# Optimization experiments

Measured on AMD Instinct MI355X. Metric: run time of the kernel, lower is better.

The kernel has to match this reference:

```python
import jax, jax.numpy as jnp
import numpy as np

B, T, D, H, O = 64, 512, 256, 1024, 1


def setup_inputs() -> dict:
    key = jax.random.key(0)
    ks = jax.random.split(key, 11)
    s_in = 1.0 / np.sqrt(H)
    def u(k, shape):
        return jax.random.uniform(k, shape, jnp.float32, -s_in, s_in)
    return {
        "x": jax.random.normal(ks[0], (B, T, D), jnp.float32),
        "w_ih_0": u(ks[1], (4 * H, D)),
        "w_hh_0": u(ks[2], (4 * H, H)),
        "b_ih_0": u(ks[3], (4 * H,)),
        "b_hh_0": u(ks[4], (4 * H,)),
        "w_ih_1": u(ks[5], (4 * H, H)),
        "w_hh_1": u(ks[6], (4 * H, H)),
        "b_ih_1": u(ks[7], (4 * H,)),
        "b_hh_1": u(ks[8], (4 * H,)),
        "w_lin": u(ks[9], (O, H)),
        "b_lin": u(ks[10], (O,)),
    }


def _lstm_layer(x, w_ih, w_hh, b_ih, b_hh):
    # x: [B, T, Din] -> h_seq: [B, T, H]. PyTorch gate order: i, f, g, o.
    # Precompute input projections for all timesteps (one big GEMM).
    xp = jnp.einsum("btd,gd->tbg", x, w_ih) + b_ih + b_hh  # [T, B, 4H]
    h0 = jnp.zeros((x.shape[0], w_hh.shape[1]), x.dtype)
    c0 = jnp.zeros_like(h0)

    def step(carry, xp_t):
        h, c = carry
        gates = xp_t + h @ w_hh.T  # [B, 4H]
        i, f, g, o = jnp.split(gates, 4, axis=-1)
        i = jax.nn.sigmoid(i)
        f = jax.nn.sigmoid(f)
        g = jnp.tanh(g)
        o = jax.nn.sigmoid(o)
        c = f * c + i * g
        h = o * jnp.tanh(c)
        return (h, c), h

    (_, _), h_seq = jax.lax.scan(step, (h0, c0), xp)  # h_seq: [T, B, H]
    return jnp.transpose(h_seq, (1, 0, 2))  # [B, T, H]


def reference(x, w_ih_0, w_hh_0, b_ih_0, b_hh_0,
              w_ih_1, w_hh_1, b_ih_1, b_hh_1, w_lin, b_lin):
    h1 = _lstm_layer(x, w_ih_0, w_hh_0, b_ih_0, b_hh_0)
    h2 = _lstm_layer(h1, w_ih_1, w_hh_1, b_ih_1, b_hh_1)
    return h2[:, -1, :] @ w_lin.T + b_lin  # [B, O]
```

## Files before the change

### kernel.cpp

```cpp
#include <hip/hip_runtime.h>


#define T_STEPS 512
#define NWG 256
#define LDS_W     131072
#define LDS_GBUF  (64 * 33 * 4)
#define LDS_CBUF  (64 * 9 * 4)
#define LDS_OFFS  (32 * 4)
#define SMEM_BYTES (LDS_W + LDS_GBUF + LDS_CBUF + LDS_OFFS)

typedef int v2i  __attribute__((ext_vector_type(2)));
typedef int v4i  __attribute__((ext_vector_type(4)));
typedef int v16i __attribute__((ext_vector_type(16)));

__device__ __forceinline__ v16i zero16() {
    v16i z;
#pragma unroll
    for (int i = 0; i < 16; ++i) z[i] = 0;
    return z;
}

__device__ __forceinline__ void load_f16_nw(const char* b0p, v4i* o) {
    const char* b1p = b0p + 4096;
    const char* b2p = b0p + 8192;
    const char* b3p = b0p + 12288;
    asm volatile(
        "global_load_dwordx4 %0, %16, off sc0 sc1\n\t"
        "global_load_dwordx4 %1, %16, off offset:16 sc0 sc1\n\t"
        "global_load_dwordx4 %2, %16, off offset:2048 sc0 sc1\n\t"
        "global_load_dwordx4 %3, %16, off offset:2064 sc0 sc1\n\t"
        "global_load_dwordx4 %4, %17, off sc0 sc1\n\t"
        "global_load_dwordx4 %5, %17, off offset:16 sc0 sc1\n\t"
        "global_load_dwordx4 %6, %17, off offset:2048 sc0 sc1\n\t"
        "global_load_dwordx4 %7, %17, off offset:2064 sc0 sc1\n\t"
        "global_load_dwordx4 %8, %18, off sc0 sc1\n\t"
        "global_load_dwordx4 %9, %18, off offset:16 sc0 sc1\n\t"
        "global_load_dwordx4 %10, %18, off offset:2048 sc0 sc1\n\t"
        "global_load_dwordx4 %11, %18, off offset:2064 sc0 sc1\n\t"
        "global_load_dwordx4 %12, %19, off sc0 sc1\n\t"
        "global_load_dwordx4 %13, %19, off offset:16 sc0 sc1\n\t"
        "global_load_dwordx4 %14, %19, off offset:2048 sc0 sc1\n\t"
        "global_load_dwordx4 %15, %19, off offset:2064 sc0 sc1"
        : "=&v"(o[0]), "=&v"(o[1]), "=&v"(o[2]), "=&v"(o[3]),
          "=&v"(o[4]), "=&v"(o[5]), "=&v"(o[6]), "=&v"(o[7]),
          "=&v"(o[8]), "=&v"(o[9]), "=&v"(o[10]), "=&v"(o[11]),
          "=&v"(o[12]), "=&v"(o[13]), "=&v"(o[14]), "=&v"(o[15])
        : "v"(b0p), "v"(b1p), "v"(b2p), "v"(b3p)
        : "memory");
}

#define WAIT_BIND(cntstr, b)                                                   \
    asm volatile("s_waitcnt vmcnt(" cntstr ")"                                 \
        : "+v"((b)[0]), "+v"((b)[1]), "+v"((b)[2]), "+v"((b)[3]),              \
          "+v"((b)[4]), "+v"((b)[5]), "+v"((b)[6]), "+v"((b)[7]),              \
          "+v"((b)[8]), "+v"((b)[9]), "+v"((b)[10]), "+v"((b)[11]),            \
          "+v"((b)[12]), "+v"((b)[13]), "+v"((b)[14]), "+v"((b)[15])           \
        :: "memory")

__device__ __forceinline__ void st16_wt(void* p, v4i v) {
    asm volatile("global_store_dwordx4 %0, %1, off sc0 sc1" :: "v"(p), "v"(v) : "memory");
}
__device__ __forceinline__ void waitcnt0() {
    asm volatile("s_waitcnt vmcnt(0)" ::: "memory");
}

__device__ __forceinline__ void split_a(v4i A0, v4i A1, v4i& HI, v4i& LO) {
    HI.x = (int)__builtin_amdgcn_perm((unsigned)A0.y, (unsigned)A0.x, 0x07050301u);
    HI.y = (int)__builtin_amdgcn_perm((unsigned)A0.w, (unsigned)A0.z, 0x07050301u);
    HI.z = (int)__builtin_amdgcn_perm((unsigned)A1.y, (unsigned)A1.x, 0x07050301u);
    HI.w = (int)__builtin_amdgcn_perm((unsigned)A1.w, (unsigned)A1.z, 0x07050301u);
    LO.x = (int)(__builtin_amdgcn_perm((unsigned)A0.y, (unsigned)A0.x, 0x06040200u) ^ 0x80808080u);
    LO.y = (int)(__builtin_amdgcn_perm((unsigned)A0.w, (unsigned)A0.z, 0x06040200u) ^ 0x80808080u);
    LO.z = (int)(__builtin_amdgcn_perm((unsigned)A1.y, (unsigned)A1.x, 0x06040200u) ^ 0x80808080u);
    LO.w = (int)(__builtin_amdgcn_perm((unsigned)A1.w, (unsigned)A1.z, 0x06040200u) ^ 0x80808080u);
}

__device__ __forceinline__ void consume8(const v4i* hb, const char* wbase,
                                         v16i& ahh, v16i& amid)
{
#pragma unroll
    for (int s = 0; s < 8; ++s) {
        v4i HI, LO; split_a(hb[2 * s], hb[2 * s + 1], HI, LO);
        v4i BH = *(const v4i*)(wbase + s * 2048);
        v4i BL = *(const v4i*)(wbase + s * 2048 + 1024);
        ahh  = __builtin_amdgcn_mfma_i32_32x32x32_i8(HI, BH, ahh, 0, 0, 0);
        amid = __builtin_amdgcn_mfma_i32_32x32x32_i8(HI, BL, amid, 0, 0, 0);
        amid = __builtin_amdgcn_mfma_i32_32x32x32_i8(LO, BH, amid, 0, 0, 0);
    }
}

__device__ __forceinline__ void kstep(const short* __restrict__ ap,
                                      const char* __restrict__ wl,
                                      v16i& ahh, v16i& amid)
{
    v4i A0 = *(const v4i*)ap;
    v4i A1 = *(const v4i*)(ap + 8);
    v4i HI, LO; split_a(A0, A1, HI, LO);
    v4i BH = *(const v4i*)wl;
    v4i BL = *(const v4i*)(wl + 1024);
    ahh  = __builtin_amdgcn_mfma_i32_32x32x32_i8(HI, BH, ahh, 0, 0, 0);
    amid = __builtin_amdgcn_mfma_i32_32x32x32_i8(HI, BL, amid, 0, 0, 0);
    amid = __builtin_amdgcn_mfma_i32_32x32x32_i8(LO, BH, amid, 0, 0, 0);
}

__global__ void quant_x(const float* __restrict__ x, short* __restrict__ xq, int n)
{
    int i = blockIdx.x * 256 + threadIdx.x;
    if (i < n) {
        float v = x[i] * 2048.f;
        v = fminf(fmaxf(v, -32767.f), 32767.f);
        xq[i] = (short)__float2int_rn(v);
    }
}

__global__ void quant_w(const float* __restrict__ wih0, const float* __restrict__ whh0,
                        const float* __restrict__ wih1, const float* __restrict__ whh1,
                        char* __restrict__ wimg)
{
    int gid = blockIdx.x * 256 + threadIdx.x;
    if (gid >= 256 * 64 * 64) return;
    int lane = gid & 63;
    int s    = (gid >> 6) & 63;
    int wg   = gid >> 12;
    int layer = wg >> 7, nblk = wg & 127;
    int col = nblk * 32 + (lane & 31);
    int ro  = (col & 3) * 1024 + (col >> 2);
    int k0  = s * 32 + (lane >> 5) * 16;
    char* dst = wimg + (size_t)wg * LDS_W + s * 2048 + lane * 16;
#pragma unroll
    for (int j = 0; j < 16; ++j) {
        int k = k0 + j;
        float w = 0.f;
        if (layer == 0) {
            if (k < 256)       w = wih0[ro * 256 + k];
            else if (k < 1280) w = whh0[ro * 1024 + (k - 256)];
        } else {
            if (k < 1024)      w = wih1[ro * 1024 + k];
            else               w = whh1[ro * 1024 + (k - 1024)];
        }
        int q  = __float2int_rn(w * 524288.f);
        int hi = (q + 128) >> 8;
        int lo = q - (hi << 8);
        dst[j]        = (char)hi;
        dst[1024 + j] = (char)lo;
    }
}

__global__ void __launch_bounds__(128) lstm_main(
    const short* __restrict__ xq, const char* __restrict__ wimg,
    const float* __restrict__ bih0, const float* __restrict__ bhh0,
    const float* __restrict__ bih1, const float* __restrict__ bhh1,
    short* __restrict__ h0q, short* __restrict__ h2q,
    float* __restrict__ h2f, unsigned* gslots, unsigned* gbcast)
{
    extern __shared__ char smem[];
    char*  wlds = smem;
    float* gbuf = (float*)(smem + LDS_W);
    float* cbuf = (float*)(smem + LDS_W + LDS_GBUF);
    float* offs = (float*)(smem + LDS_W + LDS_GBUF + LDS_CBUF);

    const int wg    = blockIdx.x;
    const int layer = wg >> 7;
    const int nblk  = wg & 127;
    const int tid   = threadIdx.x;
    const int lane  = tid & 63;
    const int RB    = tid >> 6;
    const float inv30 = 9.313225746154785e-10f;
    const float inv33 = 1.1641532182693481e-10f;

    {
        const v4i* src = (const v4i*)(wimg + (size_t)wg * LDS_W);
        v4i* dst = (v4i*)wlds;
        for (int i = tid; i < LDS_W / 16; i += 128) dst[i] = src[i];
    }
    for (int i = tid; i < 64 * 9; i += 128) cbuf[i] = 0.f;
    __syncthreads();

    if (tid < 32) {
        const int c  = tid;
        const int ns = (layer == 0) ? 40 : 64;
        int cs_x = 0, cs_h = 0;
        for (int s = 0; s < ns; ++s) {
            int sum = 0;
#pragma unroll
            for (int half = 0; half < 2; ++half) {
                const signed char* ph = (const signed char*)(wlds + s * 2048 + (half * 32 + c) * 16);
#pragma unroll
                for (int j = 0; j < 16; ++j)
                    sum += 256 * (int)ph[j] + (int)ph[1024 + j];
            }
            if (layer == 0 && s < 8) cs_x += sum; else cs_h += sum;
        }
        const int col = nblk * 32 + c;
        const int ro  = (col & 3) * 1024 + (col >> 2);
        const float bias = (layer == 0) ? (bih0[ro] + bhh0[ro]) : (bih1[ro] + bhh1[ro]);
        float off = 128.f * (float)cs_h * inv33 + bias;
        if (layer == 0) off += 128.f * (float)cs_x * inv30;
        offs[c] = off;
    }
    __syncthreads();

    const int mrow = RB * 32 + (lane & 31);
    const int ksub = (lane >> 5) * 16;
    const int j0   = nblk * 8;
    const int sj   = j0 >> 5;
    const int hbj  = (j0 >> 4) & 1;
    const int inj  = (j0 & 15) * 2;

    for (int p = 0; p <= T_STEPS; ++p) {
        const bool active = (layer == 0) ? (p < T_STEPS) : (p >= 1);

        float px[16];
        if (layer == 0 && active) {
            v16i ax = zero16(), mx = zero16();
            const short* axp = xq + ((size_t)mrow * 512 + p) * 256 + ksub;
#pragma unroll
            for (int s = 0; s < 8; ++s)
                kstep(axp + s * 32, wlds + s * 2048 + lane * 16, ax, mx);
#pragma unroll
            for (int r = 0; r < 16; ++r)
                px[r] = ((float)ax[r] * 65536.f + (float)mx[r] * 256.f) * inv30;
        }

        if (p > 0) {
            const unsigned pp = (unsigned)p;
            if (wg == 0) {
                const unsigned* s0 = gslots + (tid * 2) * 16;
                const unsigned* s1 = s0 + 16;
                while (__hip_atomic_load(s0, __ATOMIC_RELAXED, __HIP_MEMORY_SCOPE_AGENT) < pp)
                    __builtin_amdgcn_s_sleep(1);
                while (__hip_atomic_load(s1, __ATOMIC_RELAXED, __HIP_MEMORY_SCOPE_AGENT) < pp)
                    __builtin_amdgcn_s_sleep(1);
                __syncthreads();
                __hip_atomic_store(gbcast + (tid * 2) * 16, pp, __ATOMIC_RELAXED, __HIP_MEMORY_SCOPE_AGENT);
                __hip_atomic_store(gbcast + (tid * 2 + 1) * 16, pp, __ATOMIC_RELAXED, __HIP_MEMORY_SCOPE_AGENT);
            } else {
                if (tid == 0) {
                    while (__hip_atomic_load(gbcast + wg * 16, __ATOMIC_RELAXED, __HIP_MEMORY_SCOPE_AGENT) < pp)
                        __builtin_amdgcn_s_sleep(1);
                }
            }
            __syncthreads();
            asm volatile("" ::: "memory");
        }

        if (active) {
            const char* f0 = (const char*)(h0q + ((p + 1) & 1) * 65536)
                           + RB * 65536 + lane * 32;
            float gates[16];
            v16i ahh = zero16(), amid = zero16();
            v4i b0[16], b1[16];
            if (layer == 0) {
                if (p > 0) {
                    waitcnt0();
                    const char* W = wlds + lane * 16;
                    load_f16_nw(f0, b0);
                    load_f16_nw(f0 + 16384, b1);
                    WAIT_BIND("16", b0); consume8(b0, W + 8 * 2048, ahh, amid);
                    load_f16_nw(f0 + 32768, b0);
                    WAIT_BIND("16", b1); consume8(b1, W + 16 * 2048, ahh, amid);
                    load_f16_nw(f0 + 49152, b1);
                    WAIT_BIND("16", b0); consume8(b0, W + 24 * 2048, ahh, amid);
                    WAIT_BIND("0", b1);  consume8(b1, W + 32 * 2048, ahh, amid);
                }
#pragma unroll
                for (int r = 0; r < 16; ++r)
                    gates[r] = px[r]
                             + ((float)ahh[r] * 65536.f + (float)amid[r] * 256.f) * inv33
                             + offs[lane & 31];
            } else {
                const char* f2 = (const char*)(h2q + ((p + 1) & 1) * 65536)
                               + RB * 65536 + lane * 32;
                waitcnt0();
                const char* W = wlds + lane * 16;
                load_f16_nw(f0, b0);
                load_f16_nw(f0 + 16384, b1);
                WAIT_BIND("16", b0); consume8(b0, W, ahh, amid);
                load_f16_nw(f0 + 32768, b0);
                WAIT_BIND("16", b1); consume8(b1, W + 8 * 2048, ahh, amid);
                load_f16_nw(f0 + 49152, b1);
                WAIT_BIND("16", b0); consume8(b0, W + 16 * 2048, ahh, amid);
                load_f16_nw(f2, b0);
                WAIT_BIND("16", b1); consume8(b1, W + 24 * 2048, ahh, amid);
                load_f16_nw(f2 + 16384, b1);
                WAIT_BIND("16", b0); consume8(b0, W + 32 * 2048, ahh, amid);
                load_f16_nw(f2 + 32768, b0);
                WAIT_BIND("16", b1); consume8(b1, W + 40 * 2048, ahh, amid);
                load_f16_nw(f2 + 49152, b1);
                WAIT_BIND("16", b0); consume8(b0, W + 48 * 2048, ahh, amid);
                WAIT_BIND("0", b1);  consume8(b1, W + 56 * 2048, ahh, amid);
#pragma unroll
                for (int r = 0; r < 16; ++r)
                    gates[r] = ((float)ahh[r] * 65536.f + (float)amid[r] * 256.f) * inv33
                             + offs[lane & 31];
            }
            {
                const int rbase = RB * 32 + 4 * (lane >> 5);
                const int c = lane & 31;
#pragma unroll
                for (int r = 0; r < 16; ++r) {
                    int row = rbase + (r & 3) + 8 * (r >> 2);
                    gbuf[row * 33 + c] = gates[r];
                }
            }
        }
        __syncthreads();
        if (active && tid < 64) {
            const int r = tid;
            unsigned hq[8];
            float hf[8];
#pragma unroll
            for (int u = 0; u < 8; ++u) {
                const float gi = gbuf[r * 33 + 4 * u + 0];
                const float gf = gbuf[r * 33 + 4 * u + 1];
                const float gg = gbuf[r * 33 + 4 * u + 2];
                const float go = gbuf[r * 33 + 4 * u + 3];
                const float i_ = 1.f / (1.f + __expf(-gi));
                const float f_ = 1.f / (1.f + __expf(-gf));
                const float g_ = 1.f - 2.f / (__expf(2.f * gg) + 1.f);
                const float o_ = 1.f / (1.f + __expf(-go));
                float c_ = f_ * cbuf[r * 9 + u] + i_ * g_;
                cbuf[r * 9 + u] = c_;
                const float h_ = o_ * (1.f - 2.f / (__expf(2.f * c_) + 1.f));
                hq[u] = (unsigned)(unsigned short)(short)__float2int_rn(h_ * 16384.f);
                hf[u] = h_;
            }
            v4i pk;
            pk.x = (int)(hq[0] | (hq[1] << 16));
            pk.y = (int)(hq[2] | (hq[3] << 16));
            pk.z = (int)(hq[4] | (hq[5] << 16));
            pk.w = (int)(hq[6] | (hq[7] << 16));
            char* hw = (char*)(((layer == 0) ? h0q : h2q) + (p & 1) * 65536)
                     + (r >> 5) * 65536 + sj * 2048 + ((r & 31) + 32 * hbj) * 32 + inj;
            st16_wt(hw, pk);
            if (layer == 1 && p == T_STEPS) {
#pragma unroll
                for (int u = 0; u < 8; ++u) h2f[r * 1024 + j0 + u] = hf[u];
            }
        }
        if (p < T_STEPS) {
            waitcnt0();
            __syncthreads();
            if (tid == 0)
                __hip_atomic_store(gslots + wg * 16, (unsigned)(p + 1),
                                   __ATOMIC_RELAXED, __HIP_MEMORY_SCOPE_AGENT);
        }
    }
}

__global__ void final_lin(const float* __restrict__ h2f, const float* __restrict__ wlin,
                          const float* __restrict__ blin, float* __restrict__ out)
{
    const int b = blockIdx.x;
    const int l = threadIdx.x;
    float s = 0.f;
    for (int j = l; j < 1024; j += 64) s += h2f[b * 1024 + j] * wlin[j];
#pragma unroll
    for (int off = 32; off; off >>= 1) s += __shfl_down(s, off);
    if (l == 0) out[b] = s + blin[0];
}

extern "C" void kernel_launch(void* const* d_in, const int* in_sizes, int n_in,
                              void* d_out, int out_size, void* d_ws, size_t ws_size,
                              hipStream_t stream)
{
    const float* x    = (const float*)d_in[0];
    const float* wih0 = (const float*)d_in[1];
    const float* whh0 = (const float*)d_in[2];
    const float* bih0 = (const float*)d_in[3];
    const float* bhh0 = (const float*)d_in[4];
    const float* wih1 = (const float*)d_in[5];
    const float* whh1 = (const float*)d_in[6];
    const float* bih1 = (const float*)d_in[7];
    const float* bhh1 = (const float*)d_in[8];
    const float* wlin = (const float*)d_in[9];
    const float* blin = (const float*)d_in[10];

    char* ws = (char*)d_ws;
    unsigned* gslots = (unsigned*)ws;
    unsigned* gbcast = (unsigned*)(ws + 16384);
    short* h0q = (short*)(ws + 65536);
    short* h2q = (short*)(ws + 65536 + 262144);
    float* h2f = (float*)(ws + 65536 + 524288);
    short* xq  = (short*)(ws + 65536 + 786432);
    char*  wimg = ws + 65536 + 786432 + 16777216;

    hipMemsetAsync(ws, 0, 65536 + 524288, stream);

    quant_x<<<32768, 256, 0, stream>>>(x, xq, 64 * 512 * 256);
    quant_w<<<4096, 256, 0, stream>>>(wih0, whh0, wih1, whh1, wimg);

    hipFuncSetAttribute((const void*)lstm_main,
        hipFuncAttributeMaxDynamicSharedMemorySize, SMEM_BYTES);

    lstm_main<<<NWG, 128, SMEM_BYTES, stream>>>(xq, wimg, bih0, bhh0, bih1, bhh1,
                                                h0q, h2q, h2f, gslots, gbcast);
    final_lin<<<64, 64, 0, stream>>>(h2f, wlin, blin, (float*)d_out);
}
```

Measured before the change: 4.824 ms.

## Skew layer-1 by an extra step to prefetch input projection before the grid barrier

Layer 1 now lags layer 0 by two steps instead of one. Its input-projection matmul on the layer-0 hidden state is computed before the grid-wide barrier wait, and only the recurrent matmul remains after it. The layer-0 hidden-state buffer grows from double to quadruple buffering to make the extra lag safe. This takes roughly half of layer 1's post-barrier matmul off the serial critical path, at the cost of one extra loop iteration and barrier plus more workspace.

```diff
diff --git a/kernel.cpp b/kernel.cpp
--- a/kernel.cpp
+++ b/kernel.cpp
@@ -207,11 +207,15 @@
     const int hbj  = (j0 >> 4) & 1;
     const int inj  = (j0 & 15) * 2;
 
-    for (int p = 0; p <= T_STEPS; ++p) {
-        const bool active = (layer == 0) ? (p < T_STEPS) : (p >= 1);
+    for (int p = 0; p <= T_STEPS + 1; ++p) {
+        const bool actL0 = (layer == 0) && (p < T_STEPS);
+        const bool actL1 = (layer == 1) && (p >= 2);
+        const bool active = actL0 || actL1;
 
         float px[16];
-        if (layer == 0 && active) {
+        v16i ahh = zero16(), amid = zero16();
+
+        if (actL0) {
             v16i ax = zero16(), mx = zero16();
             const short* axp = xq + ((size_t)mrow * 512 + p) * 256 + ksub;
 #pragma unroll
@@ -220,6 +224,20 @@
 #pragma unroll
             for (int r = 0; r < 16; ++r)
                 px[r] = ((float)ax[r] * 65536.f + (float)mx[r] * 256.f) * inv30;
+        } else if (actL1) {
+            const char* f0 = (const char*)h0q + ((p - 2) & 3) * 131072
+                           + RB * 65536 + lane * 32;
+            v4i b0[16], b1[16];
+            waitcnt0();
+            const char* W = wlds + lane * 16;
+            load_f16_nw(f0, b0);
+            load_f16_nw(f0 + 16384, b1);
+            WAIT_BIND("16", b0); consume8(b0, W, ahh, amid);
+            load_f16_nw(f0 + 32768, b0);
+            WAIT_BIND("16", b1); consume8(b1, W + 8 * 2048, ahh, amid);
+            load_f16_nw(f0 + 49152, b1);
+            WAIT_BIND("16", b0); consume8(b0, W + 16 * 2048, ahh, amid);
+            WAIT_BIND("0", b1);  consume8(b1, W + 24 * 2048, ahh, amid);
         }
 
         if (p > 0) {
@@ -245,13 +263,12 @@
         }
 
         if (active) {
-            const char* f0 = (const char*)(h0q + ((p + 1) & 1) * 65536)
-                           + RB * 65536 + lane * 32;
             float gates[16];
-            v16i ahh = zero16(), amid = zero16();
             v4i b0[16], b1[16];
             if (layer == 0) {
                 if (p > 0) {
+                    const char* f0 = (const char*)h0q + ((p - 1) & 3) * 131072
+                                   + RB * 65536 + lane * 32;
                     waitcnt0();
                     const char* W = wlds + lane * 16;
                     load_f16_nw(f0, b0);
@@ -269,26 +286,20 @@
                              + ((float)ahh[r] * 65536.f + (float)amid[r] * 256.f) * inv33
                              + offs[lane & 31];
             } else {
-                const char* f2 = (const char*)(h2q + ((p + 1) & 1) * 65536)
-                               + RB * 65536 + lane * 32;
-                waitcnt0();
-                const char* W = wlds + lane * 16;
-                load_f16_nw(f0, b0);
-                load_f16_nw(f0 + 16384, b1);
-                WAIT_BIND("16", b0); consume8(b0, W, ahh, amid);
-                load_f16_nw(f0 + 32768, b0);
-                WAIT_BIND("16", b1); consume8(b1, W + 8 * 2048, ahh, amid);
-                load_f16_nw(f0 + 49152, b1);
-                WAIT_BIND("16", b0); consume8(b0, W + 16 * 2048, ahh, amid);
-                load_f16_nw(f2, b0);
-                WAIT_BIND("16", b1); consume8(b1, W + 24 * 2048, ahh, amid);
-                load_f16_nw(f2 + 16384, b1);
-                WAIT_BIND("16", b0); consume8(b0, W + 32 * 2048, ahh, amid);
-                load_f16_nw(f2 + 32768, b0);
-                WAIT_BIND("16", b1); consume8(b1, W + 40 * 2048, ahh, amid);
-                load_f16_nw(f2 + 49152, b1);
-                WAIT_BIND("16", b0); consume8(b0, W + 48 * 2048, ahh, amid);
-                WAIT_BIND("0", b1);  consume8(b1, W + 56 * 2048, ahh, amid);
+                if (p > 2) {
+                    const char* f2 = (const char*)h2q + ((p - 3) & 1) * 131072
+                                   + RB * 65536 + lane * 32;
+                    waitcnt0();
+                    const char* W = wlds + lane * 16;
+                    load_f16_nw(f2, b0);
+                    load_f16_nw(f2 + 16384, b1);
+                    WAIT_BIND("16", b0); consume8(b0, W + 32 * 2048, ahh, amid);
+                    load_f16_nw(f2 + 32768, b0);
+                    WAIT_BIND("16", b1); consume8(b1, W + 40 * 2048, ahh, amid);
+                    load_f16_nw(f2 + 49152, b1);
+                    WAIT_BIND("16", b0); consume8(b0, W + 48 * 2048, ahh, amid);
+                    WAIT_BIND("0", b1);  consume8(b1, W + 56 * 2048, ahh, amid);
+                }
 #pragma unroll
                 for (int r = 0; r < 16; ++r)
                     gates[r] = ((float)ahh[r] * 65536.f + (float)amid[r] * 256.f) * inv33
@@ -330,15 +341,17 @@
             pk.y = (int)(hq[2] | (hq[3] << 16));
             pk.z = (int)(hq[4] | (hq[5] << 16));
             pk.w = (int)(hq[6] | (hq[7] << 16));
-            char* hw = (char*)(((layer == 0) ? h0q : h2q) + (p & 1) * 65536)
-                     + (r >> 5) * 65536 + sj * 2048 + ((r & 31) + 32 * hbj) * 32 + inj;
+            char* hw = (layer == 0)
+                     ? (char*)h0q + (p & 3) * 131072
+                     : (char*)h2q + ((p - 2) & 1) * 131072;
+            hw += (r >> 5) * 65536 + sj * 2048 + ((r & 31) + 32 * hbj) * 32 + inj;
             st16_wt(hw, pk);
-            if (layer == 1 && p == T_STEPS) {
+            if (layer == 1 && p == T_STEPS + 1) {
 #pragma unroll
                 for (int u = 0; u < 8; ++u) h2f[r * 1024 + j0 + u] = hf[u];
             }
         }
-        if (p < T_STEPS) {
+        if (p < T_STEPS + 1) {
             waitcnt0();
             __syncthreads();
             if (tid == 0)
@@ -380,12 +393,12 @@
     unsigned* gslots = (unsigned*)ws;
     unsigned* gbcast = (unsigned*)(ws + 16384);
     short* h0q = (short*)(ws + 65536);
-    short* h2q = (short*)(ws + 65536 + 262144);
-    float* h2f = (float*)(ws + 65536 + 524288);
-    short* xq  = (short*)(ws + 65536 + 786432);
-    char*  wimg = ws + 65536 + 786432 + 16777216;
-
-    hipMemsetAsync(ws, 0, 65536 + 524288, stream);
+    short* h2q = (short*)(ws + 65536 + 524288);
+    float* h2f = (float*)(ws + 65536 + 786432);
+    short* xq  = (short*)(ws + 65536 + 1048576);
+    char*  wimg = ws + 65536 + 1048576 + 16777216;
+
+    hipMemsetAsync(ws, 0, 65536, stream);
 
     quant_x<<<32768, 256, 0, stream>>>(x, xq, 64 * 512 * 256);
     quant_w<<<4096, 256, 0, stream>>>(wih0, whh0, wih1, whh1, wimg);
```

Result: faster. 4.662 ms (-3.4%).
